# Optimization experiments

Hardware: AMD Instinct MI355X
Metric: run time of the kernel (lower is better)

The kernel has to match this reference:

```python
import jax, jax.numpy as jnp
import numpy as np
import math

N = 2048; L = 100; D_IN = 128; D_STATE = 16; D_INNER = 256
MAMBA_DIM = 128; GAT_HID = 64; HEADS = 4; GAT_OUT = 64


def _lin(key, fin, fout, scale=0.02):
    k1, k2 = jax.random.split(key)
    return (jax.random.normal(k1, (fin, fout), jnp.float32) * scale,
            jnp.zeros((fout,), jnp.float32))


def setup_inputs() -> dict:
    key = jax.random.key(0)
    ks = jax.random.split(key, 16)
    temporal_data = jax.random.normal(ks[0], (N, L, D_IN), jnp.float32)
    graph_x = jax.random.normal(ks[1], (N, D_IN), jnp.float32)
    adj = (jax.random.uniform(ks[2], (N, N)) < 0.005).astype(jnp.float32)
    adj_matrix = jnp.maximum(adj, jnp.eye(N, dtype=jnp.float32))
    pos_emb = jax.random.normal(ks[3], (1, 100, D_IN), jnp.float32)
    Wi, bi = _lin(ks[4], D_IN, D_INNER)
    Wg, bg = _lin(ks[5], D_IN, D_INNER)
    A_log = jnp.linspace(math.log(1e-3), math.log(0.1), D_STATE).reshape(1, D_STATE).astype(jnp.float32)
    Wb, bb = _lin(ks[6], D_INNER, D_STATE)
    Wc, bc = _lin(ks[7], D_IN, D_STATE)
    Wo, bo = _lin(ks[8], D_INNER, D_IN)
    Wfc, bfc = _lin(ks[9], D_IN, MAMBA_DIM)
    W1 = jax.random.normal(ks[10], (HEADS, D_IN, GAT_HID), jnp.float32) * 0.05
    a1 = jax.random.normal(ks[11], (HEADS, 2 * GAT_HID), jnp.float32) * 0.05
    W2 = jax.random.normal(ks[12], (1, HEADS * GAT_HID, GAT_OUT), jnp.float32) * 0.05
    a2 = jax.random.normal(ks[13], (1, 2 * GAT_OUT), jnp.float32) * 0.05
    return dict(temporal_data=temporal_data, graph_x=graph_x, adj_matrix=adj_matrix,
                pos_emb=pos_emb, Wi=Wi, bi=bi, Wg=Wg, bg=bg, A_log=A_log,
                Wb=Wb, bb=bb, Wc=Wc, bc=bc, Wo=Wo, bo=bo, Wfc=Wfc, bfc=bfc,
                W1=W1, a1=a1, W2=W2, a2=a2)


def _mamba(x, pos_emb, Wi, bi, Wg, bg, A_log, Wb, bb, Wc, bc, Wo, bo):
    Bt, Ls, _ = x.shape
    x = x + pos_emb[:, :Ls, :]
    x_gated = (x @ Wi + bi) * jax.nn.sigmoid(x @ Wg + bg)   # [B,L,d_inner]
    Bmat = x_gated @ Wb + bb                                 # [B,L,d_state]
    Cmat = x @ Wc + bc                                       # [B,L,d_state]
    A = jnp.exp(0.01 * jnp.exp(A_log))                       # [1,d_state] (dt=0.01)

    def step(h, bc):
        b, c = bc
        h = A * h + b
        return h, h * c

    h0 = jnp.zeros((Bt, A_log.shape[1]), x.dtype)
    _, ys = jax.lax.scan(step, h0, (jnp.swapaxes(Bmat, 0, 1), jnp.swapaxes(Cmat, 0, 1)))
    y = jnp.swapaxes(ys, 0, 1)                               # [B,L,d_state]
    d_inner = Wo.shape[0]
    out_exp = jnp.concatenate(
        [y, jnp.zeros((Bt, Ls, d_inner - y.shape[-1]), x.dtype)], axis=-1)
    return out_exp @ Wo + bo


def _gat_layer(x, adj, W, a, concat):
    # x: [N,Fin], W: [H,Fin,Fout], a: [H,2*Fout]
    F_out = W.shape[2]
    xt = jnp.einsum('nf,hfo->hno', x, W)                     # [H,N,Fout]
    e_src = jnp.einsum('hno,ho->hn', xt, a[:, :F_out])       # a . x_i part
    e_dst = jnp.einsum('hno,ho->hn', xt, a[:, F_out:])       # a . x_j part
    e = jax.nn.leaky_relu(e_src[:, :, None] + e_dst[:, None, :], 0.2)
    e = jnp.where(adj[None, :, :] > 0, e, -jnp.inf)
    att = jax.nn.softmax(e, axis=2)                          # masked entries -> 0
    h_prime = jnp.einsum('hij,hjo->hio', att, xt)            # [H,N,Fout]
    if concat:
        return jnp.transpose(h_prime, (1, 0, 2)).reshape(x.shape[0], -1)
    return h_prime.mean(axis=0)


def reference(temporal_data, graph_x, adj_matrix, pos_emb, Wi, bi, Wg, bg, A_log,
              Wb, bb, Wc, bc, Wo, bo, Wfc, bfc, W1, a1, W2, a2):
    mamba_out = _mamba(temporal_data, pos_emb, Wi, bi, Wg, bg, A_log, Wb, bb, Wc, bc, Wo, bo)
    mamba_features = mamba_out @ Wfc + bfc
    # GAT stack (dropout is identity in eval mode)
    h = _gat_layer(graph_x, adj_matrix, W1, a1, concat=True)
    h = jax.nn.relu(h)
    gat_features = _gat_layer(h, adj_matrix, W2, a2, concat=False)
    return mamba_features, gat_features
```

## Files before the change

### kernel.cpp

```cpp
#include <hip/hip_runtime.h>
#include <hip/hip_bf16.h>

#define N_NODES 2048
#define L_SEQ   100
#define ROWS    (N_NODES * L_SEQ)
#define HEADS   4
#define GHID    64

typedef __attribute__((ext_vector_type(8))) short bf16x8;
typedef __attribute__((ext_vector_type(4))) float floatx4;

__device__ __forceinline__ short f2bf(float f) {
    union { float f; unsigned u; } v; v.f = f;
    return (short)((v.u + 0x8000u) >> 16);
}

constexpr size_t OFF_WCOMB = 0;
constexpr size_t OFF_BCOMB = 2048;
constexpr size_t OFF_AEXP  = 2176;
constexpr size_t OFF_WIGS  = 2192;
constexpr size_t OFF_WBS   = 34960;
constexpr size_t OFF_WCS   = 37008;
constexpr size_t OFF_BM    = 38032;
constexpr size_t OFF_CM    = OFF_BM + (size_t)ROWS * 16;
constexpr size_t OFF_XT1   = OFF_BM;
constexpr size_t OFF_ES1   = OFF_XT1 + (size_t)HEADS * N_NODES * GHID;
constexpr size_t OFF_ED1   = OFF_ES1 + HEADS * N_NODES;
constexpr size_t OFF_H1    = OFF_ED1 + HEADS * N_NODES;
constexpr size_t OFF_XT2   = OFF_H1 + (size_t)N_NODES * 256;
constexpr size_t OFF_ES2   = OFF_XT2 + (size_t)N_NODES * 64;
constexpr size_t OFF_ED2   = OFF_ES2 + N_NODES;

__global__ void k0_comb(const float* __restrict__ Wo, const float* __restrict__ bo,
                        const float* __restrict__ Wfc, const float* __restrict__ bfc,
                        const float* __restrict__ A_log, float* __restrict__ ws) {
    const int b = blockIdx.x, f2 = threadIdx.x;
    if (b < 16) {
        float a = 0.f;
        for (int f = 0; f < 128; f++) a += Wo[b * 128 + f] * Wfc[f * 128 + f2];
        ws[OFF_WCOMB + b * 128 + f2] = a;
    } else {
        float acc = bfc[f2];
        for (int f = 0; f < 128; f++) acc += bo[f] * Wfc[f * 128 + f2];
        ws[OFF_BCOMB + f2] = acc;
        if (f2 < 16) ws[OFF_AEXP + f2] = expf(0.01f * expf(A_log[f2]));
    }
}

__global__ void k0_prep(const float* __restrict__ Wi, const float* __restrict__ Wg,
                        const float* __restrict__ Wb, const float* __restrict__ Wc,
                        float* __restrict__ ws) {
    int i = blockIdx.x * 256 + threadIdx.x;
    short* wigs = (short*)(ws + OFF_WIGS);
    short* wbs  = (short*)(ws + OFF_WBS);
    short* wcs  = (short*)(ws + OFF_WCS);
    if (i < 65536) {
        int j = i & 7, lane = (i >> 3) & 63, ks = (i >> 9) & 3, nt = i >> 11;
        int w = nt >> 3, t = nt & 7;
        int col = w * 64 + (t & 3) * 16 + (lane & 15);
        int k   = ks * 32 + (lane >> 4) * 8 + j;
        float v = (t < 4) ? Wi[k * 256 + col] : Wg[k * 256 + col];
        wigs[i] = f2bf(v);
    } else if (i < 65536 + 4096) {
        int ii = i - 65536;
        int j = ii & 7, lane = (ii >> 3) & 63, ks = ii >> 9;
        int k = ks * 32 + (lane >> 4) * 8 + j, n = lane & 15;
        wbs[ii] = f2bf(Wb[k * 16 + n]);
    } else if (i < 65536 + 4096 + 2048) {
        int ii = i - 65536 - 4096;
        int j = ii & 7, lane = (ii >> 3) & 63, ks = ii >> 9;
        int k = ks * 32 + (lane >> 4) * 8 + j, n = lane & 15;
        wcs[ii] = f2bf(Wc[k * 16 + n]);
    }
}

__global__ __launch_bounds__(512, 4) void k1_mfma(
    const float* __restrict__ temporal, const float* __restrict__ pos,
    const float* __restrict__ bi, const float* __restrict__ bg,
    const float* __restrict__ bb, const float* __restrict__ bc,
    const float* __restrict__ ws, float* __restrict__ Bm, float* __restrict__ Cm) {
    __shared__ short xbf[64][136];
    __shared__ short gbf[64][264];
    const int tid = threadIdx.x, wave = tid >> 6, lane = tid & 63;
    const int m = lane & 15, quad = lane >> 4;
    const int r0 = blockIdx.x * 64;
    const int l0 = r0 % L_SEQ;

#pragma unroll
    for (int i = 0; i < 4; i++) {
        int f4  = i * 512 + tid;
        int row = f4 >> 5;
        int c4  = (f4 & 31) * 4;
        int l = l0 + row; if (l >= L_SEQ) l -= L_SEQ;
        float4 tv = *(const float4*)(temporal + (size_t)(r0 + row) * 128 + c4);
        float4 pv = *(const float4*)(pos + l * 128 + c4);
        short4 sv;
        sv.x = f2bf(tv.x + pv.x); sv.y = f2bf(tv.y + pv.y);
        sv.z = f2bf(tv.z + pv.z); sv.w = f2bf(tv.w + pv.w);
        *(short4*)&xbf[row][c4] = sv;
    }
    __syncthreads();

    const short* Wigs = (const short*)(ws + OFF_WIGS);
    const int wg = wave >> 1, wp = wave & 1;
    floatx4 acc[4][4] = {};
#pragma unroll
    for (int ks = 0; ks < 4; ks++) {
        bf16x8 bfr[4];
#pragma unroll
        for (int jl = 0; jl < 4; jl++) {
            int ntg = wg * 8 + wp * 2 + (jl & 1) + ((jl >> 1) << 2);
            bfr[jl] = *(const bf16x8*)(Wigs + (size_t)((ntg * 4 + ks) * 64 + lane) * 8);
        }
        bf16x8 afr[4];
#pragma unroll
        for (int mt = 0; mt < 4; mt++)
            afr[mt] = *(const bf16x8*)&xbf[mt * 16 + m][ks * 32 + quad * 8];
#pragma unroll
        for (int mt = 0; mt < 4; mt++)
#pragma unroll
            for (int jl = 0; jl < 4; jl++)
                acc[mt][jl] = __builtin_amdgcn_mfma_f32_16x16x32_bf16(
                    afr[mt], bfr[jl], acc[mt][jl], 0, 0, 0);
    }

    const float NL2E = -1.44269504f;
#pragma unroll
    for (int tp = 0; tp < 2; tp++) {
        int col = wave * 32 + tp * 16 + m;
        float biv = bi[col];
        float bgs = bg[col] * NL2E;
#pragma unroll
        for (int mt = 0; mt < 4; mt++) {
#pragma unroll
            for (int r = 0; r < 4; r++) {
                float li = acc[mt][tp][r] + biv;
                float ex = __builtin_amdgcn_exp2f(fmaf(acc[mt][tp + 2][r], NL2E, bgs));
                float g  = li * __builtin_amdgcn_rcpf(1.f + ex);
                gbf[mt * 16 + quad * 4 + r][col] = f2bf(g);
            }
        }
    }
    __syncthreads();

    if (wave < 4) {
        const short* Wbs = (const short*)(ws + OFF_WBS);
        floatx4 accB = {};
#pragma unroll
        for (int ks = 0; ks < 8; ks++) {
            bf16x8 a = *(const bf16x8*)&gbf[wave * 16 + m][ks * 32 + quad * 8];
            bf16x8 b = *(const bf16x8*)(Wbs + (size_t)(ks * 64 + lane) * 8);
            accB = __builtin_amdgcn_mfma_f32_16x16x32_bf16(a, b, accB, 0, 0, 0);
        }
        float bbv = bb[m];
#pragma unroll
        for (int r = 0; r < 4; r++) {
            int row = r0 + wave * 16 + quad * 4 + r;
            Bm[(size_t)row * 16 + m] = accB[r] + bbv;
        }
    } else {
        const short* Wcs = (const short*)(ws + OFF_WCS);
        const int mt = wave - 4;
        floatx4 accC = {};
#pragma unroll
        for (int ks = 0; ks < 4; ks++) {
            bf16x8 a = *(const bf16x8*)&xbf[mt * 16 + m][ks * 32 + quad * 8];
            bf16x8 b = *(const bf16x8*)(Wcs + (size_t)(ks * 64 + lane) * 8);
            accC = __builtin_amdgcn_mfma_f32_16x16x32_bf16(a, b, accC, 0, 0, 0);
        }
        float bcv = bc[m];
#pragma unroll
        for (int r = 0; r < 4; r++) {
            int row = r0 + mt * 16 + quad * 4 + r;
            Cm[(size_t)row * 16 + m] = accC[r] + bcv;
        }
    }
}

__global__ __launch_bounds__(128) void k2_scan(const float* __restrict__ ws,
                                               float* __restrict__ out) {
    __shared__ float sb[1600], sc[1600];
    const int n = blockIdx.x, f = threadIdx.x;
    const float4* Bm4 = (const float4*)(ws + OFF_BM + (size_t)n * 1600);
    const float4* Cm4 = (const float4*)(ws + OFF_CM + (size_t)n * 1600);
#pragma unroll
    for (int i = 0; i < 4; i++) {
        int idx = i * 128 + f;
        if (idx < 400) {
            ((float4*)sb)[idx] = Bm4[idx];
            ((float4*)sc)[idx] = Cm4[idx];
        }
    }
    float w[16], A[16], h[16];
#pragma unroll
    for (int s = 0; s < 16; s++) {
        w[s] = ws[OFF_WCOMB + s * 128 + f];
        A[s] = ws[OFF_AEXP + s];
        h[s] = 0.f;
    }
    const float bcb = ws[OFF_BCOMB + f];
    __syncthreads();
    for (int l = 0; l < L_SEQ; l++) {
        float acc = bcb;
#pragma unroll
        for (int s = 0; s < 16; s++) {
            h[s] = A[s] * h[s] + sb[l * 16 + s];
            acc += h[s] * sc[l * 16 + s] * w[s];
        }
        out[((size_t)n * L_SEQ + l) * 128 + f] = acc;
    }
}

__global__ __launch_bounds__(64) void k4_xt1(const float* __restrict__ gx,
                                             const float* __restrict__ W1,
                                             const float* __restrict__ a1,
                                             float* __restrict__ ws) {
    const int b = blockIdx.x;
    const int h = b >> 11;
    const int n = b & 2047;
    const int o = threadIdx.x;
    float acc = 0.f;
    for (int f = 0; f < 128; f++)
        acc += gx[n * 128 + f] * W1[(h * 128 + f) * 64 + o];
    ws[OFF_XT1 + ((size_t)h * 2048 + n) * 64 + o] = acc;
    float es = acc * a1[h * 128 + o];
    float ed = acc * a1[h * 128 + 64 + o];
#pragma unroll
    for (int off = 32; off > 0; off >>= 1) {
        es += __shfl_down(es, off);
        ed += __shfl_down(ed, off);
    }
    if (o == 0) { ws[OFF_ES1 + h * 2048 + n] = es; ws[OFF_ED1 + h * 2048 + n] = ed; }
}

__global__ __launch_bounds__(256) void k5_att1(const float* __restrict__ adj,
                                               const float* __restrict__ ws,
                                               float* __restrict__ h1out) {
    __shared__ int list[2048];
    __shared__ int cnt;
    const int n = blockIdx.x, tid = threadIdx.x;
    if (tid == 0) cnt = 0;
    __syncthreads();
    for (int j = tid; j < 2048; j += 256)
        if (adj[(size_t)n * 2048 + j] > 0.f) list[atomicAdd(&cnt, 1)] = j;
    __syncthreads();
    const int h = tid >> 6, o = tid & 63;
    const float  es = ws[OFF_ES1 + h * 2048 + n];
    const float* ed = ws + OFF_ED1 + h * 2048;
    const float* xt = ws + OFF_XT1 + (size_t)h * 2048 * 64;
    float num = 0.f, den = 0.f;
    const int mm = cnt;
    for (int ii = 0; ii < mm; ii++) {
        int j = list[ii];
        float e = es + ed[j];
        e = (e > 0.f) ? e : 0.2f * e;
        float wgt = expf(e);
        den += wgt;
        num += wgt * xt[(size_t)j * 64 + o];
    }
    float v = num / den;
    h1out[(size_t)n * 256 + h * 64 + o] = v > 0.f ? v : 0.f;
}

__global__ __launch_bounds__(64) void k6_xt2(const float* __restrict__ W2,
                                             const float* __restrict__ a2,
                                             float* __restrict__ ws) {
    const int n = blockIdx.x, o = threadIdx.x;
    const float* h1 = ws + OFF_H1 + (size_t)n * 256;
    float acc = 0.f;
    for (int f = 0; f < 256; f++) acc += h1[f] * W2[f * 64 + o];
    ws[OFF_XT2 + (size_t)n * 64 + o] = acc;
    float es = acc * a2[o];
    float ed = acc * a2[64 + o];
#pragma unroll
    for (int off = 32; off > 0; off >>= 1) {
        es += __shfl_down(es, off);
        ed += __shfl_down(ed, off);
    }
    if (o == 0) { ws[OFF_ES2 + n] = es; ws[OFF_ED2 + n] = ed; }
}

__global__ __launch_bounds__(64) void k7_att2(const float* __restrict__ adj,
                                              const float* __restrict__ ws,
                                              float* __restrict__ gout) {
    __shared__ int list[2048];
    __shared__ int cnt;
    const int n = blockIdx.x, o = threadIdx.x;
    if (o == 0) cnt = 0;
    __syncthreads();
    for (int j = o; j < 2048; j += 64)
        if (adj[(size_t)n * 2048 + j] > 0.f) list[atomicAdd(&cnt, 1)] = j;
    __syncthreads();
    const float es = ws[OFF_ES2 + n];
    float num = 0.f, den = 0.f;
    const int mm = cnt;
    for (int ii = 0; ii < mm; ii++) {
        int j = list[ii];
        float e = es + ws[OFF_ED2 + j];
        e = (e > 0.f) ? e : 0.2f * e;
        float wgt = expf(e);
        den += wgt;
        num += wgt * ws[OFF_XT2 + (size_t)j * 64 + o];
    }
    gout[(size_t)n * 64 + o] = num / den;
}

extern "C" void kernel_launch(void* const* d_in, const int* in_sizes, int n_in,
                              void* d_out, int out_size, void* d_ws, size_t ws_size,
                              hipStream_t stream) {
    const float* temporal = (const float*)d_in[0];
    const float* graph_x  = (const float*)d_in[1];
    const float* adj      = (const float*)d_in[2];
    const float* pos      = (const float*)d_in[3];
    const float* Wi  = (const float*)d_in[4];
    const float* bi  = (const float*)d_in[5];
    const float* Wg  = (const float*)d_in[6];
    const float* bg  = (const float*)d_in[7];
    const float* A_log = (const float*)d_in[8];
    const float* Wb  = (const float*)d_in[9];
    const float* bb  = (const float*)d_in[10];
    const float* Wc  = (const float*)d_in[11];
    const float* bc  = (const float*)d_in[12];
    const float* Wo  = (const float*)d_in[13];
    const float* bo  = (const float*)d_in[14];
    const float* Wfc = (const float*)d_in[15];
    const float* bfc = (const float*)d_in[16];
    const float* W1  = (const float*)d_in[17];
    const float* a1  = (const float*)d_in[18];
    const float* W2  = (const float*)d_in[19];
    const float* a2  = (const float*)d_in[20];

    float* ws = (float*)d_ws;
    float* out_mamba = (float*)d_out;
    float* out_gat   = out_mamba + (size_t)ROWS * 128;

    k0_comb<<<17, 128, 0, stream>>>(Wo, bo, Wfc, bfc, A_log, ws);
    k0_prep<<<280, 256, 0, stream>>>(Wi, Wg, Wb, Wc, ws);
    k1_mfma<<<ROWS / 64, 512, 0, stream>>>(temporal, pos, bi, bg, bb, bc, ws,
                                           ws + OFF_BM, ws + OFF_CM);
    k2_scan<<<N_NODES, 128, 0, stream>>>(ws, out_mamba);
    k4_xt1<<<HEADS * N_NODES, 64, 0, stream>>>(graph_x, W1, a1, ws);
    k5_att1<<<N_NODES, 256, 0, stream>>>(adj, ws, ws + OFF_H1);
    k6_xt2<<<N_NODES, 64, 0, stream>>>(W2, a2, ws);
    k7_att2<<<N_NODES, 64, 0, stream>>>(adj, ws, out_gat);
}
```

Measured before the change: 353.2 us.

## Merge prep kernels, fuse GAT attention with second projection, widen small-block kernels

After: 327.9 us. 1.08x faster.

```diff
diff --git a/kernel.cpp b/kernel.cpp
--- a/kernel.cpp
+++ b/kernel.cpp
@@ -31,26 +31,33 @@
 constexpr size_t OFF_ES2   = OFF_XT2 + (size_t)N_NODES * 64;
 constexpr size_t OFF_ED2   = OFF_ES2 + N_NODES;
 
-__global__ void k0_comb(const float* __restrict__ Wo, const float* __restrict__ bo,
-                        const float* __restrict__ Wfc, const float* __restrict__ bfc,
-                        const float* __restrict__ A_log, float* __restrict__ ws) {
-    const int b = blockIdx.x, f2 = threadIdx.x;
-    if (b < 16) {
-        float a = 0.f;
-        for (int f = 0; f < 128; f++) a += Wo[b * 128 + f] * Wfc[f * 128 + f2];
-        ws[OFF_WCOMB + b * 128 + f2] = a;
-    } else {
-        float acc = bfc[f2];
-        for (int f = 0; f < 128; f++) acc += bo[f] * Wfc[f * 128 + f2];
-        ws[OFF_BCOMB + f2] = acc;
-        if (f2 < 16) ws[OFF_AEXP + f2] = expf(0.01f * expf(A_log[f2]));
-    }
-}
-
-__global__ void k0_prep(const float* __restrict__ Wi, const float* __restrict__ Wg,
-                        const float* __restrict__ Wb, const float* __restrict__ Wc,
-                        float* __restrict__ ws) {
-    int i = blockIdx.x * 256 + threadIdx.x;
+__global__ __launch_bounds__(256) void kA_prep(
+    const float* __restrict__ Wo, const float* __restrict__ bo,
+    const float* __restrict__ Wfc, const float* __restrict__ bfc,
+    const float* __restrict__ A_log,
+    const float* __restrict__ Wi, const float* __restrict__ Wg,
+    const float* __restrict__ Wb, const float* __restrict__ Wc,
+    float* __restrict__ ws) {
+    const int b = blockIdx.x;
+    if (b < 9) {
+        int i = b * 256 + threadIdx.x;
+        if (i < 2048) {
+            int row = i >> 7, col = i & 127;
+            float a = 0.f;
+            for (int f = 0; f < 128; f++) a += Wo[row * 128 + f] * Wfc[f * 128 + col];
+            ws[OFF_WCOMB + i] = a;
+        } else if (i < 2176) {
+            int col = i - 2048;
+            float acc = bfc[col];
+            for (int f = 0; f < 128; f++) acc += bo[f] * Wfc[f * 128 + col];
+            ws[OFF_BCOMB + col] = acc;
+        } else if (i < 2192) {
+            int s = i - 2176;
+            ws[OFF_AEXP + s] = expf(0.01f * expf(A_log[s]));
+        }
+        return;
+    }
+    int i = (b - 9) * 256 + threadIdx.x;
     short* wigs = (short*)(ws + OFF_WIGS);
     short* wbs  = (short*)(ws + OFF_WBS);
     short* wcs  = (short*)(ws + OFF_WCS);
@@ -177,18 +184,19 @@
     }
 }
 
-__global__ __launch_bounds__(128) void k2_scan(const float* __restrict__ ws,
+__global__ __launch_bounds__(256) void k2_scan(const float* __restrict__ ws,
                                                float* __restrict__ out) {
-    __shared__ float sb[1600], sc[1600];
-    const int n = blockIdx.x, f = threadIdx.x;
+    __shared__ float sb[2][1600], sc[2][1600];
+    const int sub = threadIdx.x >> 7, f = threadIdx.x & 127;
+    const int n = blockIdx.x * 2 + sub;
     const float4* Bm4 = (const float4*)(ws + OFF_BM + (size_t)n * 1600);
     const float4* Cm4 = (const float4*)(ws + OFF_CM + (size_t)n * 1600);
 #pragma unroll
     for (int i = 0; i < 4; i++) {
         int idx = i * 128 + f;
         if (idx < 400) {
-            ((float4*)sb)[idx] = Bm4[idx];
-            ((float4*)sc)[idx] = Cm4[idx];
+            ((float4*)sb[sub])[idx] = Bm4[idx];
+            ((float4*)sc[sub])[idx] = Cm4[idx];
         }
     }
     float w[16], A[16], h[16];
@@ -200,25 +208,30 @@
     }
     const float bcb = ws[OFF_BCOMB + f];
     __syncthreads();
+    const float* sbn = sb[sub];
+    const float* scn = sc[sub];
     for (int l = 0; l < L_SEQ; l++) {
-        float acc = bcb;
-#pragma unroll
-        for (int s = 0; s < 16; s++) {
-            h[s] = A[s] * h[s] + sb[l * 16 + s];
-            acc += h[s] * sc[l * 16 + s] * w[s];
-        }
-        out[((size_t)n * L_SEQ + l) * 128 + f] = acc;
-    }
-}
-
-__global__ __launch_bounds__(64) void k4_xt1(const float* __restrict__ gx,
-                                             const float* __restrict__ W1,
-                                             const float* __restrict__ a1,
-                                             float* __restrict__ ws) {
-    const int b = blockIdx.x;
-    const int h = b >> 11;
-    const int n = b & 2047;
-    const int o = threadIdx.x;
+        float acc0 = bcb, acc1 = 0.f;
+#pragma unroll
+        for (int s = 0; s < 8; s++) {
+            h[s] = A[s] * h[s] + sbn[l * 16 + s];
+            acc0 += h[s] * scn[l * 16 + s] * w[s];
+        }
+#pragma unroll
+        for (int s = 8; s < 16; s++) {
+            h[s] = A[s] * h[s] + sbn[l * 16 + s];
+            acc1 += h[s] * scn[l * 16 + s] * w[s];
+        }
+        out[((size_t)n * L_SEQ + l) * 128 + f] = acc0 + acc1;
+    }
+}
+
+__global__ __launch_bounds__(256) void k4_xt1(const float* __restrict__ gx,
+                                              const float* __restrict__ W1,
+                                              const float* __restrict__ a1,
+                                              float* __restrict__ ws) {
+    const int n = blockIdx.x;
+    const int h = threadIdx.x >> 6, o = threadIdx.x & 63;
     float acc = 0.f;
     for (int f = 0; f < 128; f++)
         acc += gx[n * 128 + f] * W1[(h * 128 + f) * 64 + o];
@@ -233,11 +246,14 @@
     if (o == 0) { ws[OFF_ES1 + h * 2048 + n] = es; ws[OFF_ED1 + h * 2048 + n] = ed; }
 }
 
-__global__ __launch_bounds__(256) void k5_att1(const float* __restrict__ adj,
-                                               const float* __restrict__ ws,
-                                               float* __restrict__ h1out) {
+__global__ __launch_bounds__(256) void k56_att1(const float* __restrict__ adj,
+                                                const float* __restrict__ W2,
+                                                const float* __restrict__ a2,
+                                                float* __restrict__ ws) {
     __shared__ int list[2048];
     __shared__ int cnt;
+    __shared__ float sh1[256];
+    __shared__ float sred[4][64];
     const int n = blockIdx.x, tid = threadIdx.x;
     if (tid == 0) cnt = 0;
     __syncthreads();
@@ -245,56 +261,66 @@
         if (adj[(size_t)n * 2048 + j] > 0.f) list[atomicAdd(&cnt, 1)] = j;
     __syncthreads();
     const int h = tid >> 6, o = tid & 63;
-    const float  es = ws[OFF_ES1 + h * 2048 + n];
-    const float* ed = ws + OFF_ED1 + h * 2048;
-    const float* xt = ws + OFF_XT1 + (size_t)h * 2048 * 64;
-    float num = 0.f, den = 0.f;
-    const int mm = cnt;
-    for (int ii = 0; ii < mm; ii++) {
-        int j = list[ii];
-        float e = es + ed[j];
-        e = (e > 0.f) ? e : 0.2f * e;
-        float wgt = expf(e);
-        den += wgt;
-        num += wgt * xt[(size_t)j * 64 + o];
-    }
-    float v = num / den;
-    h1out[(size_t)n * 256 + h * 64 + o] = v > 0.f ? v : 0.f;
-}
-
-__global__ __launch_bounds__(64) void k6_xt2(const float* __restrict__ W2,
-                                             const float* __restrict__ a2,
-                                             float* __restrict__ ws) {
-    const int n = blockIdx.x, o = threadIdx.x;
-    const float* h1 = ws + OFF_H1 + (size_t)n * 256;
-    float acc = 0.f;
-    for (int f = 0; f < 256; f++) acc += h1[f] * W2[f * 64 + o];
-    ws[OFF_XT2 + (size_t)n * 64 + o] = acc;
-    float es = acc * a2[o];
-    float ed = acc * a2[64 + o];
-#pragma unroll
-    for (int off = 32; off > 0; off >>= 1) {
-        es += __shfl_down(es, off);
-        ed += __shfl_down(ed, off);
-    }
-    if (o == 0) { ws[OFF_ES2 + n] = es; ws[OFF_ED2 + n] = ed; }
-}
-
-__global__ __launch_bounds__(64) void k7_att2(const float* __restrict__ adj,
-                                              const float* __restrict__ ws,
-                                              float* __restrict__ gout) {
+    {
+        const float  es = ws[OFF_ES1 + h * 2048 + n];
+        const float* ed = ws + OFF_ED1 + h * 2048;
+        const float* xt = ws + OFF_XT1 + (size_t)h * 2048 * 64;
+        float num = 0.f, den = 0.f;
+        const int mm = cnt;
+        for (int ii = 0; ii < mm; ii++) {
+            int j = list[ii];
+            float e = es + ed[j];
+            e = (e > 0.f) ? e : 0.2f * e;
+            float wgt = expf(e);
+            den += wgt;
+            num += wgt * xt[(size_t)j * 64 + o];
+        }
+        float v = num / den;
+        sh1[h * 64 + o] = v > 0.f ? v : 0.f;
+    }
+    __syncthreads();
+    {
+        const int g = h, o2 = o;
+        float part = 0.f;
+        const int f0 = g * 64;
+#pragma unroll 8
+        for (int f = 0; f < 64; f++)
+            part += sh1[f0 + f] * W2[(f0 + f) * 64 + o2];
+        sred[g][o2] = part;
+    }
+    __syncthreads();
+    if (tid < 64) {
+        float xt2v = sred[0][tid] + sred[1][tid] + sred[2][tid] + sred[3][tid];
+        ws[OFF_XT2 + (size_t)n * 64 + tid] = xt2v;
+        float es = xt2v * a2[tid];
+        float ed = xt2v * a2[64 + tid];
+#pragma unroll
+        for (int off = 32; off > 0; off >>= 1) {
+            es += __shfl_down(es, off);
+            ed += __shfl_down(ed, off);
+        }
+        if (tid == 0) { ws[OFF_ES2 + n] = es; ws[OFF_ED2 + n] = ed; }
+    }
+}
+
+__global__ __launch_bounds__(256) void k7_att2(const float* __restrict__ adj,
+                                               const float* __restrict__ ws,
+                                               float* __restrict__ gout) {
     __shared__ int list[2048];
     __shared__ int cnt;
-    const int n = blockIdx.x, o = threadIdx.x;
-    if (o == 0) cnt = 0;
-    __syncthreads();
-    for (int j = o; j < 2048; j += 64)
+    __shared__ float snum[4][64];
+    __shared__ float sden[4];
+    const int n = blockIdx.x, tid = threadIdx.x;
+    const int g = tid >> 6, o = tid & 63;
+    if (tid == 0) cnt = 0;
+    __syncthreads();
+    for (int j = tid; j < 2048; j += 256)
         if (adj[(size_t)n * 2048 + j] > 0.f) list[atomicAdd(&cnt, 1)] = j;
     __syncthreads();
     const float es = ws[OFF_ES2 + n];
     float num = 0.f, den = 0.f;
     const int mm = cnt;
-    for (int ii = 0; ii < mm; ii++) {
+    for (int ii = g; ii < mm; ii += 4) {
         int j = list[ii];
         float e = es + ws[OFF_ED2 + j];
         e = (e > 0.f) ? e : 0.2f * e;
@@ -302,7 +328,14 @@
         den += wgt;
         num += wgt * ws[OFF_XT2 + (size_t)j * 64 + o];
     }
-    gout[(size_t)n * 64 + o] = num / den;
+    snum[g][o] = num;
+    if (o == 0) sden[g] = den;
+    __syncthreads();
+    if (tid < 64) {
+        float nt = snum[0][tid] + snum[1][tid] + snum[2][tid] + snum[3][tid];
+        float dt = sden[0] + sden[1] + sden[2] + sden[3];
+        gout[(size_t)n * 64 + tid] = nt / dt;
+    }
 }
 
 extern "C" void kernel_launch(void* const* d_in, const int* in_sizes, int n_in,
@@ -334,13 +367,11 @@
     float* out_mamba = (float*)d_out;
     float* out_gat   = out_mamba + (size_t)ROWS * 128;
 
-    k0_comb<<<17, 128, 0, stream>>>(Wo, bo, Wfc, bfc, A_log, ws);
-    k0_prep<<<280, 256, 0, stream>>>(Wi, Wg, Wb, Wc, ws);
+    kA_prep<<<289, 256, 0, stream>>>(Wo, bo, Wfc, bfc, A_log, Wi, Wg, Wb, Wc, ws);
     k1_mfma<<<ROWS / 64, 512, 0, stream>>>(temporal, pos, bi, bg, bb, bc, ws,
                                            ws + OFF_BM, ws + OFF_CM);
-    k2_scan<<<N_NODES, 128, 0, stream>>>(ws, out_mamba);
-    k4_xt1<<<HEADS * N_NODES, 64, 0, stream>>>(graph_x, W1, a1, ws);
-    k5_att1<<<N_NODES, 256, 0, stream>>>(adj, ws, ws + OFF_H1);
-    k6_xt2<<<N_NODES, 64, 0, stream>>>(W2, a2, ws);
-    k7_att2<<<N_NODES, 64, 0, stream>>>(adj, ws, out_gat);
-}
+    k2_scan<<<N_NODES / 2, 256, 0, stream>>>(ws, out_mamba);
+    k4_xt1<<<N_NODES, 256, 0, stream>>>(graph_x, W1, a1, ws);
+    k56_att1<<<N_NODES, 256, 0, stream>>>(adj, W2, a2, ws);
+    k7_att2<<<N_NODES, 256, 0, stream>>>(adj, ws, out_gat);
+}
```
